# Performance work log

Measured on AMD Instinct MI355X. Metric: run time of the kernel, lower is better.

## Reference

```python
import jax, jax.numpy as jnp
import numpy as np

IN_DIM = 768
N_HEADS = 12
HEAD_DIM = IN_DIM // N_HEADS


def setup_inputs() -> dict:
    key = jax.random.key(0)
    k1, k2, k3, k4, k5 = jax.random.split(key, 5)
    x = jax.random.normal(k1, (2, 2048, IN_DIM), dtype=jnp.float32)
    s = 1.0 / np.sqrt(IN_DIM)
    W_qkv = jax.random.uniform(k2, (IN_DIM, 3 * IN_DIM), jnp.float32, -s, s)
    b_qkv = jax.random.uniform(k3, (3 * IN_DIM,), jnp.float32, -s, s)
    W_out = jax.random.uniform(k4, (IN_DIM, IN_DIM), jnp.float32, -s, s)
    b_out = jax.random.uniform(k5, (IN_DIM,), jnp.float32, -s, s)
    return {"x": x, "W_qkv": W_qkv, "b_qkv": b_qkv, "W_out": W_out, "b_out": b_out}


def reference(x, W_qkv, b_qkv, W_out, b_out):
    B, N, D = x.shape
    qkv = x @ W_qkv + b_qkv  # [B, N, 3D]
    qkv = qkv.reshape(B, N, 3, N_HEADS, HEAD_DIM)
    qkv = jnp.transpose(qkv, (2, 0, 3, 1, 4))  # [3, B, H, N, Dh]
    q, k, v = qkv[0], qkv[1], qkv[2]
    scale = 1.0 / np.sqrt(HEAD_DIM)
    scores = jnp.einsum("bhqd,bhkd->bhqk", q, k) * scale  # [B, H, N, N]
    attn = jax.nn.softmax(scores, axis=-1)
    out = jnp.einsum("bhqk,bhkd->bhqd", attn, v)  # [B, H, N, Dh]
    out = jnp.transpose(out, (0, 2, 1, 3)).reshape(B, N, D)
    return out @ W_out + b_out
```

## Files before the change

kernel.cpp:

```cpp
#include <hip/hip_runtime.h>

#define DEVI __device__ __forceinline__

typedef __attribute__((ext_vector_type(8))) short short8;
typedef __attribute__((ext_vector_type(4))) short s16x4;
typedef __attribute__((ext_vector_type(4))) float f32x4;
typedef __attribute__((ext_vector_type(16))) float f32x16;

DEVI unsigned short f32_to_bf16(float f) {
  unsigned int u = __float_as_uint(f);
  u += 0x7fffu + ((u >> 16) & 1u);
  return (unsigned short)(u >> 16);
}
DEVI float bf16_to_f32(unsigned short h) {
  return __uint_as_float(((unsigned int)h) << 16);
}

DEVI void gld_lds16(const void* g, void* l) {
  __builtin_amdgcn_global_load_lds(
      (__attribute__((address_space(1))) void*)(g),
      (__attribute__((address_space(3))) void*)(l), 16, 0, 0);
}

__global__ __launch_bounds__(256) void k_prep(const float* __restrict__ x,
                                              const float* __restrict__ Wq,
                                              const float* __restrict__ Wo,
                                              unsigned short* __restrict__ Xb,
                                              unsigned short* __restrict__ Wq_t,
                                              unsigned short* __restrict__ Wo_t) {
  int blk = blockIdx.x;
  int tid = threadIdx.x;
  if (blk < 1536) {
    int i = blk * 256 + tid;
    const float* src = x + (size_t)i * 8;
    short8 v;
#pragma unroll
    for (int j = 0; j < 8; ++j) v[j] = (short)f32_to_bf16(src[j]);
    *(short8*)&Xb[(size_t)i * 8] = v;
    return;
  }
  const float* W;
  unsigned short* Wt;
  int kt, nt, K, N;
  if (blk < 3264) {
    int idx = blk - 1536;
    kt = idx % 24;
    nt = idx / 24;
    W = Wq;
    Wt = Wq_t;
    K = 768;
    N = 2304;
  } else {
    int idx = blk - 3264;
    kt = idx % 24;
    nt = idx / 24;
    W = Wo;
    Wt = Wo_t;
    K = 768;
    N = 768;
  }
  __shared__ float t[32][33];
#pragma unroll
  for (int p = 0; p < 4; ++p) {
    int idx = tid + p * 256;
    int rr = idx >> 5, cc = idx & 31;
    t[rr][cc] = W[(size_t)(kt * 32 + rr) * N + nt * 32 + cc];
  }
  __syncthreads();
#pragma unroll
  for (int p = 0; p < 4; ++p) {
    int idx = tid + p * 256;
    int rn = idx >> 5, ck = idx & 31;
    Wt[(size_t)(nt * 32 + rn) * K + kt * 32 + ck] = f32_to_bf16(t[ck][rn]);
  }
}

__global__ __launch_bounds__(256) void k_gemm_qkv(const unsigned short* __restrict__ A,
                                                  const unsigned short* __restrict__ Bt,
                                                  const float* __restrict__ bias,
                                                  int M, int N, int K,
                                                  unsigned short* __restrict__ Qo,
                                                  unsigned short* __restrict__ Ko,
                                                  unsigned short* __restrict__ Vt) {
  __shared__ __align__(16) unsigned short As[128 * 32];
  __shared__ __align__(16) unsigned short Bs[64 * 32];
  int tid = threadIdx.x;
  int tm = blockIdx.x, tn = blockIdx.y;
  int lane = tid & 63, wid = tid >> 6;
  int g = lane >> 4, lr = lane & 15;
  f32x4 acc[2][4] = {};
  int srow = tid >> 2;
  int scol = (tid & 3) * 8;
  const unsigned short* Ab = A + (size_t)tm * 128 * K;
  const unsigned short* Bb = Bt + (size_t)tn * 64 * K;
  for (int k0 = 0; k0 < K; k0 += 32) {
    gld_lds16(Ab + (size_t)srow * K + k0 + scol, &As[srow * 32 + scol]);
    gld_lds16(Ab + (size_t)(srow + 64) * K + k0 + scol, &As[(srow + 64) * 32 + scol]);
    gld_lds16(Bb + (size_t)srow * K + k0 + scol, &Bs[srow * 32 + scol]);
    __syncthreads();
    short8 a[2], b[4];
#pragma unroll
    for (int m = 0; m < 2; ++m)
      a[m] = *(const short8*)&As[(wid * 32 + m * 16 + lr) * 32 + g * 8];
#pragma unroll
    for (int n = 0; n < 4; ++n)
      b[n] = *(const short8*)&Bs[(n * 16 + lr) * 32 + g * 8];
#pragma unroll
    for (int m = 0; m < 2; ++m)
#pragma unroll
      for (int n = 0; n < 4; ++n)
        acc[m][n] = __builtin_amdgcn_mfma_f32_16x16x32_bf16(a[m], b[n], acc[m][n], 0, 0, 0);
    __syncthreads();
  }
  const float QSCALE = 0.125f * 1.4426950408889634f;
  int sec = tn / 12;
  int cb = tn * 64 - sec * 768;
#pragma unroll
  for (int m = 0; m < 2; ++m) {
#pragma unroll
    for (int n = 0; n < 4; ++n) {
      int c = cb + n * 16 + lr;
      int hh = c >> 6, d = c & 63;
      float bv = bias[tn * 64 + n * 16 + lr];
      int rowb = tm * 128 + wid * 32 + m * 16 + g * 4;
      int bb = rowb >> 11, nn = rowb & 2047;
      int bh = bb * 12 + hh;
      if (sec == 2) {
        s16x4 v4;
#pragma unroll
        for (int j = 0; j < 4; ++j) v4[j] = (short)f32_to_bf16(acc[m][n][j] + bv);
        *(s16x4*)&Vt[((size_t)bh * 64 + d) * 2048 + nn] = v4;
      } else {
        unsigned short* dst0 = (sec == 0) ? Qo : Ko;
        float sc = (sec == 0) ? QSCALE : 1.0f;
#pragma unroll
        for (int j = 0; j < 4; ++j) {
          size_t dst = (((size_t)bh << 11) + nn + j) * 64 + d;
          dst0[dst] = f32_to_bf16((acc[m][n][j] + bv) * sc);
        }
      }
    }
  }
}

__global__ __launch_bounds__(256) void k_gemm2(const unsigned short* __restrict__ A,
                                               const unsigned short* __restrict__ Bt,
                                               const float* __restrict__ bias,
                                               float* __restrict__ C,
                                               int M, int N, int K) {
  __shared__ __align__(16) unsigned short As[64 * 32];
  __shared__ __align__(16) unsigned short Bs[64 * 32];
  int tid = threadIdx.x;
  int tm = blockIdx.x, tn = blockIdx.y;
  int lane = tid & 63, wid = tid >> 6;
  int wr = wid >> 1, wc = wid & 1;
  int g = lane >> 4, lr = lane & 15;
  f32x4 acc[2][2] = {};
  int srow = tid >> 2;
  int scol = (tid & 3) * 8;
  const unsigned short* Ab = A + (size_t)tm * 64 * K;
  const unsigned short* Bb = Bt + (size_t)tn * 64 * K;
  for (int k0 = 0; k0 < K; k0 += 32) {
    gld_lds16(Ab + (size_t)srow * K + k0 + scol, &As[srow * 32 + scol]);
    gld_lds16(Bb + (size_t)srow * K + k0 + scol, &Bs[srow * 32 + scol]);
    __syncthreads();
    short8 a[2], b[2];
#pragma unroll
    for (int m = 0; m < 2; ++m)
      a[m] = *(const short8*)&As[(wr * 32 + m * 16 + lr) * 32 + g * 8];
#pragma unroll
    for (int n = 0; n < 2; ++n)
      b[n] = *(const short8*)&Bs[(wc * 32 + n * 16 + lr) * 32 + g * 8];
#pragma unroll
    for (int m = 0; m < 2; ++m)
#pragma unroll
      for (int n = 0; n < 2; ++n)
        acc[m][n] = __builtin_amdgcn_mfma_f32_16x16x32_bf16(a[m], b[n], acc[m][n], 0, 0, 0);
    __syncthreads();
  }
#pragma unroll
  for (int m = 0; m < 2; ++m) {
#pragma unroll
    for (int n = 0; n < 2; ++n) {
      int col = tn * 64 + wc * 32 + n * 16 + lr;
      float bv = bias[col];
#pragma unroll
      for (int j = 0; j < 4; ++j) {
        int row = tm * 64 + wr * 32 + m * 16 + g * 4 + j;
        C[(size_t)row * N + col] = acc[m][n][j] + bv;
      }
    }
  }
}


#define ATTN_STAGE(KSB, VSB, T)                                                          \
  {                                                                                      \
    int kv0 = (T) * 64;                                                                  \
    _Pragma("unroll") for (int it = 0; it < 2; ++it) {                                   \
      int L = tid + it * 256;                                                            \
      int rw = L >> 3, s7 = L & 7;                                                       \
      gld_lds16(Kb + (size_t)(khead + kv0 + rw) * 64 + ((s7 ^ (rw & 7)) * 8),            \
                &KSB[L * 8]);                                                            \
      gld_lds16(Vt + (size_t)(vhead + rw) * 2048 + kv0 + ((s7 ^ (rw & 7)) * 8),          \
                &VSB[L * 8]);                                                            \
    }                                                                                    \
  }

#define BUILD_PA(S)                                                                      \
  {                                                                                      \
    unsigned int b0, a0, e0, c0;                                                         \
    asm("v_cvt_pk_bf16_f32 %0, %1, %2" : "=v"(b0) : "v"(S[0]), "v"(S[1]));               \
    asm("v_cvt_pk_bf16_f32 %0, %1, %2" : "=v"(a0) : "v"(S[4]), "v"(S[5]));               \
    asm("v_permlane32_swap_b32 %0, %1" : "+v"(b0), "+v"(a0));                            \
    asm("v_cvt_pk_bf16_f32 %0, %1, %2" : "=v"(e0) : "v"(S[2]), "v"(S[3]));               \
    asm("v_cvt_pk_bf16_f32 %0, %1, %2" : "=v"(c0) : "v"(S[6]), "v"(S[7]));               \
    asm("v_permlane32_swap_b32 %0, %1" : "+v"(e0), "+v"(c0));                            \
    paw[0][0] = b0; paw[0][1] = e0; paw[0][2] = a0; paw[0][3] = c0;                      \
    unsigned int b1, a1, e1, c1;                                                         \
    asm("v_cvt_pk_bf16_f32 %0, %1, %2" : "=v"(b1) : "v"(S[8]), "v"(S[9]));               \
    asm("v_cvt_pk_bf16_f32 %0, %1, %2" : "=v"(a1) : "v"(S[12]), "v"(S[13]));             \
    asm("v_permlane32_swap_b32 %0, %1" : "+v"(b1), "+v"(a1));                            \
    asm("v_cvt_pk_bf16_f32 %0, %1, %2" : "=v"(e1) : "v"(S[10]), "v"(S[11]));             \
    asm("v_cvt_pk_bf16_f32 %0, %1, %2" : "=v"(c1) : "v"(S[14]), "v"(S[15]));             \
    asm("v_permlane32_swap_b32 %0, %1" : "+v"(e1), "+v"(c1));                            \
    paw[1][0] = b1; paw[1][1] = e1; paw[1][2] = a1; paw[1][3] = c1;                      \
  }

#define PROC_TILE(KSB, VSB)                                                              \
  {                                                                                      \
    f32x16 sa = {};                                                                      \
    __builtin_amdgcn_s_setprio(1);                                                       \
    _Pragma("unroll") for (int ds = 0; ds < 4; ++ds) {                                   \
      short8 kf = *(const short8*)&KSB[(kh * 32 + ln31) * 64 + (((ds * 2 + hi) ^ ln7) * 8)]; \
      sa = __builtin_amdgcn_mfma_f32_32x32x16_bf16(kf, qf[ds], sa, 0, 0, 0);             \
    }                                                                                    \
    __builtin_amdgcn_s_setprio(0);                                                       \
    _Pragma("unroll") for (int i = 0; i < 16; ++i) {                                     \
      float pv = exp2f(sa[i]);                                                           \
      sa[i] = pv;                                                                        \
      lrun += pv;                                                                        \
    }                                                                                    \
    unsigned int paw[2][4];                                                              \
    BUILD_PA(sa)                                                                         \
    __builtin_amdgcn_s_setprio(1);                                                       \
    _Pragma("unroll") for (int kl = 0; kl < 2; ++kl) {                                   \
      union {                                                                            \
        unsigned int u[4];                                                               \
        short8 s8;                                                                      \
      } pu;                                                                              \
      pu.u[0] = paw[kl][0];                                                              \
      pu.u[1] = paw[kl][1];                                                              \
      pu.u[2] = paw[kl][2];                                                              \
      pu.u[3] = paw[kl][3];                                                              \
      int ksg = kh * 2 + kl;                                                             \
      short8 vb0 = *(const short8*)&VSB[ln31 * 64 + (((ksg * 2 + hi) ^ ln7) * 8)];       \
      short8 vb1 = *(const short8*)&VSB[(32 + ln31) * 64 + (((ksg * 2 + hi) ^ ln7) * 8)]; \
      oacc0 = __builtin_amdgcn_mfma_f32_32x32x16_bf16(pu.s8, vb0, oacc0, 0, 0, 0);       \
      oacc1 = __builtin_amdgcn_mfma_f32_32x32x16_bf16(pu.s8, vb1, oacc1, 0, 0, 0);       \
    }                                                                                    \
    __builtin_amdgcn_s_setprio(0);                                                       \
  }

__global__ __launch_bounds__(256, 4) void k_attn(const unsigned short* __restrict__ Qb,
                                                 const unsigned short* __restrict__ Kb,
                                                 const unsigned short* __restrict__ Vt,
                                                 unsigned short* __restrict__ Xh) {
  int bh = blockIdx.x;
  int qb = blockIdx.y;
  int b = bh / 12, h = bh - b * 12;
  __shared__ __align__(16) unsigned short LDSbuf[4 * 64 * 64];
  unsigned short* Ks0 = LDSbuf;
  unsigned short* Vs0 = LDSbuf + 64 * 64;
  unsigned short* Ks1 = LDSbuf + 2 * 64 * 64;
  unsigned short* Vs1 = LDSbuf + 3 * 64 * 64;
  int tid = threadIdx.x;
  int wid = tid >> 6, lane = tid & 63;
  int qh = wid >> 1, kh = wid & 1;
  int ln31 = lane & 31, hi = lane >> 5, ln7 = lane & 7;
  int khead = bh * 2048;
  int vhead = bh * 64;
  int q0 = qb * 64 + qh * 32;

  short8 qf[4];
#pragma unroll
  for (int ds = 0; ds < 4; ++ds)
    qf[ds] = *(const short8*)&Qb[(size_t)(khead + q0 + ln31) * 64 + ds * 16 + hi * 8];

  float lrun = 0.f;
  f32x16 oacc0 = {}, oacc1 = {};

  ATTN_STAGE(Ks0, Vs0, 0);
  __syncthreads();
#pragma unroll 1
  for (int tt = 0; tt < 16; ++tt) {
    ATTN_STAGE(Ks1, Vs1, 2 * tt + 1);
    PROC_TILE(Ks0, Vs0);
    __syncthreads();
    if (tt < 15) ATTN_STAGE(Ks0, Vs0, 2 * tt + 2);
    PROC_TILE(Ks1, Vs1);
    __syncthreads();
  }

  lrun += __shfl_xor(lrun, 32, 64);

  float* scr = (float*)LDSbuf;
  if (kh == 1) {
    float* p = scr + (size_t)(qh * 64 + lane) * 33;
#pragma unroll
    for (int i = 0; i < 16; ++i) {
      p[i] = oacc0[i];
      p[16 + i] = oacc1[i];
    }
    p[32] = lrun;
  }
  __syncthreads();
  if (kh == 0) {
    float* p = scr + (size_t)(qh * 64 + lane) * 33;
#pragma unroll
    for (int i = 0; i < 16; ++i) {
      oacc0[i] += p[i];
      oacc1[i] += p[16 + i];
    }
    lrun += p[32];
    float linv = 1.0f / lrun;
#pragma unroll
    for (int r = 0; r < 16; ++r) {
      int qrow = (r & 3) + 8 * (r >> 2) + 4 * hi;
      float lf = __shfl(linv, qrow, 64);
      int grow = b * 2048 + q0 + qrow;
      int colb = h * 64 + ln31;
      Xh[(size_t)grow * 768 + colb] = f32_to_bf16(oacc0[r] * lf);
      Xh[(size_t)grow * 768 + colb + 32] = f32_to_bf16(oacc1[r] * lf);
    }
  }
}

extern "C" void kernel_launch(void* const* d_in, const int* in_sizes, int n_in,
                              void* d_out, int out_size, void* d_ws, size_t ws_size,
                              hipStream_t stream) {
  const float* x = (const float*)d_in[0];
  const float* W_qkv = (const float*)d_in[1];
  const float* b_qkv = (const float*)d_in[2];
  const float* W_out = (const float*)d_in[3];
  const float* b_out = (const float*)d_in[4];
  float* out = (float*)d_out;
  char* ws = (char*)d_ws;

  unsigned short* Xh = (unsigned short*)(ws + 0);
  unsigned short* Xb = (unsigned short*)(ws + 18874368);
  unsigned short* Wq_t = (unsigned short*)(ws + 25165824);
  unsigned short* Wo_t = (unsigned short*)(ws + 28704768);
  unsigned short* Qb = (unsigned short*)(ws + 32243712);
  unsigned short* Kb = (unsigned short*)(ws + 38535168);
  unsigned short* Vt = (unsigned short*)(ws + 51118080);

  k_prep<<<3840, 256, 0, stream>>>(x, W_qkv, W_out, Xb, Wq_t, Wo_t);
  k_gemm_qkv<<<dim3(32, 36), 256, 0, stream>>>(Xb, Wq_t, b_qkv, 4096, 2304, 768, Qb, Kb, Vt);
  k_attn<<<dim3(24, 32), 256, 0, stream>>>(Qb, Kb, Vt, Xh);
  k_gemm2<<<dim3(64, 12), 256, 0, stream>>>(Xh, Wo_t, b_out, out, 4096, 768, 768);
}
```

Before: 95.57 us.

## Split attention key range across two blocks and merge partial outputs

The attention kernel now runs with a z-dimension of 2, each block handling half of the key tiles and writing unnormalized bf16 partial outputs plus row sums. A new merge kernel adds the two partials and divides by the combined sum to produce the head output. This doubles the number of attention blocks (768 to 1536) to improve occupancy across CUs. In exchange it adds an extra kernel launch, extra global traffic for the partials, and rounds the unnormalized partials to bf16 before the merge. There is no max subtraction and the softmax relies on exp2 of the raw scores, so the split is exact only because both halves share the same (zero) offset.

```diff
diff --git a/kernel.cpp b/kernel.cpp
--- a/kernel.cpp
+++ b/kernel.cpp
@@ -247,7 +247,7 @@
     _Pragma("unroll") for (int kl = 0; kl < 2; ++kl) {                                   \
       union {                                                                            \
         unsigned int u[4];                                                               \
-        short8 s8;                                                                      \
+        short8 s8;                                                                       \
       } pu;                                                                              \
       pu.u[0] = paw[kl][0];                                                              \
       pu.u[1] = paw[kl][1];                                                              \
@@ -265,10 +265,13 @@
 __global__ __launch_bounds__(256, 4) void k_attn(const unsigned short* __restrict__ Qb,
                                                  const unsigned short* __restrict__ Kb,
                                                  const unsigned short* __restrict__ Vt,
-                                                 unsigned short* __restrict__ Xh) {
+                                                 unsigned short* __restrict__ Op0,
+                                                 unsigned short* __restrict__ Op1,
+                                                 float* __restrict__ Lout) {
   int bh = blockIdx.x;
   int qb = blockIdx.y;
-  int b = bh / 12, h = bh - b * 12;
+  int z = blockIdx.z;
+  int b = bh / 12;
   __shared__ __align__(16) unsigned short LDSbuf[4 * 64 * 64];
   unsigned short* Ks0 = LDSbuf;
   unsigned short* Vs0 = LDSbuf + 64 * 64;
@@ -281,6 +284,7 @@
   int khead = bh * 2048;
   int vhead = bh * 64;
   int q0 = qb * 64 + qh * 32;
+  int t0 = z * 16;
 
   short8 qf[4];
 #pragma unroll
@@ -290,14 +294,14 @@
   float lrun = 0.f;
   f32x16 oacc0 = {}, oacc1 = {};
 
-  ATTN_STAGE(Ks0, Vs0, 0);
+  ATTN_STAGE(Ks0, Vs0, t0);
   __syncthreads();
 #pragma unroll 1
-  for (int tt = 0; tt < 16; ++tt) {
-    ATTN_STAGE(Ks1, Vs1, 2 * tt + 1);
+  for (int tt = 0; tt < 8; ++tt) {
+    ATTN_STAGE(Ks1, Vs1, t0 + 2 * tt + 1);
     PROC_TILE(Ks0, Vs0);
     __syncthreads();
-    if (tt < 15) ATTN_STAGE(Ks0, Vs0, 2 * tt + 2);
+    if (tt < 7) ATTN_STAGE(Ks0, Vs0, t0 + 2 * tt + 2);
     PROC_TILE(Ks1, Vs1);
     __syncthreads();
   }
@@ -323,17 +327,43 @@
       oacc1[i] += p[16 + i];
     }
     lrun += p[32];
-    float linv = 1.0f / lrun;
+    unsigned short* Op = z ? Op1 : Op0;
+    int h = bh - b * 12;
 #pragma unroll
     for (int r = 0; r < 16; ++r) {
       int qrow = (r & 3) + 8 * (r >> 2) + 4 * hi;
-      float lf = __shfl(linv, qrow, 64);
       int grow = b * 2048 + q0 + qrow;
       int colb = h * 64 + ln31;
-      Xh[(size_t)grow * 768 + colb] = f32_to_bf16(oacc0[r] * lf);
-      Xh[(size_t)grow * 768 + colb + 32] = f32_to_bf16(oacc1[r] * lf);
-    }
-  }
+      Op[(size_t)grow * 768 + colb] = f32_to_bf16(oacc0[r]);
+      Op[(size_t)grow * 768 + colb + 32] = f32_to_bf16(oacc1[r]);
+    }
+    if (hi == 0) Lout[((size_t)z * 24 + bh) * 2048 + q0 + ln31] = lrun;
+  }
+}
+
+__global__ __launch_bounds__(256) void k_merge(const unsigned short* __restrict__ Op0,
+                                               const unsigned short* __restrict__ Op1,
+                                               const float* __restrict__ Lbuf,
+                                               unsigned short* __restrict__ Xh) {
+  int idx = blockIdx.x * 256 + threadIdx.x;
+  int row = idx / 96;
+  int c0 = (idx - row * 96) * 8;
+  int b = row >> 11, n = row & 2047;
+  int h = c0 >> 6;
+  int bh = b * 12 + h;
+  float l0 = Lbuf[((size_t)0 * 24 + bh) * 2048 + n];
+  float l1 = Lbuf[((size_t)1 * 24 + bh) * 2048 + n];
+  float inv = 1.0f / (l0 + l1);
+  size_t base = (size_t)row * 768 + c0;
+  short8 o0 = *(const short8*)&Op0[base];
+  short8 o1 = *(const short8*)&Op1[base];
+  short8 w;
+#pragma unroll
+  for (int j = 0; j < 8; ++j) {
+    float v = (bf16_to_f32((unsigned short)o0[j]) + bf16_to_f32((unsigned short)o1[j])) * inv;
+    w[j] = (short)f32_to_bf16(v);
+  }
+  *(short8*)&Xh[base] = w;
 }
 
 extern "C" void kernel_launch(void* const* d_in, const int* in_sizes, int n_in,
@@ -353,10 +383,14 @@
   unsigned short* Wo_t = (unsigned short*)(ws + 28704768);
   unsigned short* Qb = (unsigned short*)(ws + 32243712);
   unsigned short* Kb = (unsigned short*)(ws + 38535168);
+  unsigned short* Op0 = (unsigned short*)(ws + 44826624);
   unsigned short* Vt = (unsigned short*)(ws + 51118080);
+  unsigned short* Op1 = (unsigned short*)(ws + 57409536);
+  float* Lbuf = (float*)(ws + 63700992);
 
   k_prep<<<3840, 256, 0, stream>>>(x, W_qkv, W_out, Xb, Wq_t, Wo_t);
   k_gemm_qkv<<<dim3(32, 36), 256, 0, stream>>>(Xb, Wq_t, b_qkv, 4096, 2304, 768, Qb, Kb, Vt);
-  k_attn<<<dim3(24, 32), 256, 0, stream>>>(Qb, Kb, Vt, Xh);
+  k_attn<<<dim3(24, 32, 2), 256, 0, stream>>>(Qb, Kb, Vt, Op0, Op1, Lbuf);
+  k_merge<<<1536, 256, 0, stream>>>(Op0, Op1, Lbuf, Xh);
   k_gemm2<<<dim3(64, 12), 256, 0, stream>>>(Xh, Wo_t, b_out, out, 4096, 768, 768);
 }
```

New measurement: 99.80 us. 4.4% more time.

## Load K/V fragments directly from global into registers, drop LDS staging

Applied to the files above, without the earlier changes.

Replaces the LDS double-buffered K/V staging (global_load_lds plus barriers) with direct per-wave global loads of the MFMA fragments into registers, double-buffered in registers across tiles. This removes the per-tile __syncthreads and LDS traffic. Each wave now loads only the data it needs, and within a block the two waves sharing a kh half request the same K/V data instead of staging it once through LDS. The launch-bounds occupancy hint is also dropped, and register pressure rises from holding two fragment sets, which may lower occupancy.

```diff
diff --git a/kernel.cpp b/kernel.cpp
--- a/kernel.cpp
+++ b/kernel.cpp
@@ -194,16 +194,17 @@
 }
 
 
-#define ATTN_STAGE(KSB, VSB, T)                                                          \
+#define LOAD_KV(KF, VB, T)                                                               \
   {                                                                                      \
     int kv0 = (T) * 64;                                                                  \
-    _Pragma("unroll") for (int it = 0; it < 2; ++it) {                                   \
-      int L = tid + it * 256;                                                            \
-      int rw = L >> 3, s7 = L & 7;                                                       \
-      gld_lds16(Kb + (size_t)(khead + kv0 + rw) * 64 + ((s7 ^ (rw & 7)) * 8),            \
-                &KSB[L * 8]);                                                            \
-      gld_lds16(Vt + (size_t)(vhead + rw) * 2048 + kv0 + ((s7 ^ (rw & 7)) * 8),          \
-                &VSB[L * 8]);                                                            \
+    const unsigned short* kr =                                                           \
+        Kb + (size_t)(khead + kv0 + kh * 32 + ln31) * 64 + hi * 8;                       \
+    _Pragma("unroll") for (int ds = 0; ds < 4; ++ds)                                     \
+        KF[ds] = *(const short8*)(kr + ds * 16);                                         \
+    _Pragma("unroll") for (int kl = 0; kl < 2; ++kl) {                                   \
+      int col = kv0 + ((kh * 2 + kl) * 2 + hi) * 8;                                      \
+      VB[kl][0] = *(const short8*)&Vt[(size_t)(vhead + ln31) * 2048 + col];              \
+      VB[kl][1] = *(const short8*)&Vt[(size_t)(vhead + 32 + ln31) * 2048 + col];         \
     }                                                                                    \
   }
 
@@ -227,14 +228,12 @@
     paw[1][0] = b1; paw[1][1] = e1; paw[1][2] = a1; paw[1][3] = c1;                      \
   }
 
-#define PROC_TILE(KSB, VSB)                                                              \
+#define PROC(KF, VB)                                                                     \
   {                                                                                      \
     f32x16 sa = {};                                                                      \
     __builtin_amdgcn_s_setprio(1);                                                       \
-    _Pragma("unroll") for (int ds = 0; ds < 4; ++ds) {                                   \
-      short8 kf = *(const short8*)&KSB[(kh * 32 + ln31) * 64 + (((ds * 2 + hi) ^ ln7) * 8)]; \
-      sa = __builtin_amdgcn_mfma_f32_32x32x16_bf16(kf, qf[ds], sa, 0, 0, 0);             \
-    }                                                                                    \
+    _Pragma("unroll") for (int ds = 0; ds < 4; ++ds)                                     \
+        sa = __builtin_amdgcn_mfma_f32_32x32x16_bf16(KF[ds], qf[ds], sa, 0, 0, 0);       \
     __builtin_amdgcn_s_setprio(0);                                                       \
     _Pragma("unroll") for (int i = 0; i < 16; ++i) {                                     \
       float pv = exp2f(sa[i]);                                                           \
@@ -247,37 +246,30 @@
     _Pragma("unroll") for (int kl = 0; kl < 2; ++kl) {                                   \
       union {                                                                            \
         unsigned int u[4];                                                               \
-        short8 s8;                                                                      \
+        short8 s8;                                                                       \
       } pu;                                                                              \
       pu.u[0] = paw[kl][0];                                                              \
       pu.u[1] = paw[kl][1];                                                              \
       pu.u[2] = paw[kl][2];                                                              \
       pu.u[3] = paw[kl][3];                                                              \
-      int ksg = kh * 2 + kl;                                                             \
-      short8 vb0 = *(const short8*)&VSB[ln31 * 64 + (((ksg * 2 + hi) ^ ln7) * 8)];       \
-      short8 vb1 = *(const short8*)&VSB[(32 + ln31) * 64 + (((ksg * 2 + hi) ^ ln7) * 8)]; \
-      oacc0 = __builtin_amdgcn_mfma_f32_32x32x16_bf16(pu.s8, vb0, oacc0, 0, 0, 0);       \
-      oacc1 = __builtin_amdgcn_mfma_f32_32x32x16_bf16(pu.s8, vb1, oacc1, 0, 0, 0);       \
+      oacc0 = __builtin_amdgcn_mfma_f32_32x32x16_bf16(pu.s8, VB[kl][0], oacc0, 0, 0, 0); \
+      oacc1 = __builtin_amdgcn_mfma_f32_32x32x16_bf16(pu.s8, VB[kl][1], oacc1, 0, 0, 0); \
     }                                                                                    \
     __builtin_amdgcn_s_setprio(0);                                                       \
   }
 
-__global__ __launch_bounds__(256, 4) void k_attn(const unsigned short* __restrict__ Qb,
-                                                 const unsigned short* __restrict__ Kb,
-                                                 const unsigned short* __restrict__ Vt,
-                                                 unsigned short* __restrict__ Xh) {
+__global__ __launch_bounds__(256) void k_attn(const unsigned short* __restrict__ Qb,
+                                              const unsigned short* __restrict__ Kb,
+                                              const unsigned short* __restrict__ Vt,
+                                              unsigned short* __restrict__ Xh) {
   int bh = blockIdx.x;
   int qb = blockIdx.y;
   int b = bh / 12, h = bh - b * 12;
-  __shared__ __align__(16) unsigned short LDSbuf[4 * 64 * 64];
-  unsigned short* Ks0 = LDSbuf;
-  unsigned short* Vs0 = LDSbuf + 64 * 64;
-  unsigned short* Ks1 = LDSbuf + 2 * 64 * 64;
-  unsigned short* Vs1 = LDSbuf + 3 * 64 * 64;
+  __shared__ float scr[2 * 64 * 33];
   int tid = threadIdx.x;
   int wid = tid >> 6, lane = tid & 63;
   int qh = wid >> 1, kh = wid & 1;
-  int ln31 = lane & 31, hi = lane >> 5, ln7 = lane & 7;
+  int ln31 = lane & 31, hi = lane >> 5;
   int khead = bh * 2048;
   int vhead = bh * 64;
   int q0 = qb * 64 + qh * 32;
@@ -290,21 +282,19 @@
   float lrun = 0.f;
   f32x16 oacc0 = {}, oacc1 = {};
 
-  ATTN_STAGE(Ks0, Vs0, 0);
-  __syncthreads();
+  short8 kfA[4], kfB[4];
+  short8 vbA[2][2], vbB[2][2];
+  LOAD_KV(kfA, vbA, 0)
 #pragma unroll 1
   for (int tt = 0; tt < 16; ++tt) {
-    ATTN_STAGE(Ks1, Vs1, 2 * tt + 1);
-    PROC_TILE(Ks0, Vs0);
-    __syncthreads();
-    if (tt < 15) ATTN_STAGE(Ks0, Vs0, 2 * tt + 2);
-    PROC_TILE(Ks1, Vs1);
-    __syncthreads();
+    LOAD_KV(kfB, vbB, 2 * tt + 1)
+    PROC(kfA, vbA)
+    if (tt < 15) LOAD_KV(kfA, vbA, 2 * tt + 2)
+    PROC(kfB, vbB)
   }
 
   lrun += __shfl_xor(lrun, 32, 64);
 
-  float* scr = (float*)LDSbuf;
   if (kh == 1) {
     float* p = scr + (size_t)(qh * 64 + lane) * 33;
 #pragma unroll
```

New measurement: 141.5 us. 1.48x slower.
